# Kernel optimization log

Measured on AMD Instinct MI355X. Metric: run time of the kernel, lower is better.

Reference implementation:

```python
import jax, jax.numpy as jnp
import numpy as np

N, E, D, R, L = 50000, 600000, 64, 65, 2


def setup_inputs() -> dict:
    key = jax.random.key(0)
    ks = jax.random.split(key, 10)
    x = jax.random.normal(ks[0], (N, D), dtype=jnp.float32)
    edge_index = jax.random.randint(ks[1], (2, E), 0, N, dtype=jnp.int64)
    edge_type = jax.random.randint(ks[2], (E,), 0, R, dtype=jnp.int64)
    s = 1.0 / np.sqrt(D)
    W = jax.random.normal(ks[3], (L, R, D, D), dtype=jnp.float32) * s
    root = jax.random.normal(ks[4], (L, D, D), dtype=jnp.float32) * s
    bias = jax.random.normal(ks[5], (L, D), dtype=jnp.float32) * 0.01
    res_W = jax.random.normal(ks[6], (L, D, D), dtype=jnp.float32) * s
    res_b = jax.random.normal(ks[7], (L, D), dtype=jnp.float32) * 0.01
    return {"x": x, "edge_index": edge_index, "edge_type": edge_type,
            "W": W, "root": root, "bias": bias, "res_W": res_W, "res_b": res_b}


def _rgcn_conv(x, src, dst, edge_type, W_r, W_root, b):
    # PyG RGCNConv (num_bases=None, aggr='mean'):
    #   out_i = x_i @ W_root + b + sum_r mean_{j in N_r(i)} (x_j @ W_r)
    # mean is linear, so aggregate raw features per (node, relation) first,
    # then apply the per-relation transform once per node.
    n, d = x.shape
    r = W_r.shape[0]
    seg = dst * r + edge_type                       # [E]
    msg = x[src]                                    # [E, D] gather
    agg = jax.ops.segment_sum(msg, seg, num_segments=n * r).reshape(n, r, d)
    cnt = jax.ops.segment_sum(jnp.ones((msg.shape[0],), x.dtype), seg,
                              num_segments=n * r).reshape(n, r, 1)
    mean = agg / jnp.maximum(cnt, 1.0)              # [N, R, D]
    out = jnp.einsum('nrd,rdk->nk', mean, W_r)
    return out + x @ W_root + b


def reference(x, edge_index, edge_type, W, root, bias, res_W, res_b):
    src, dst = edge_index[0], edge_index[1]
    h = x
    for l in range(W.shape[0]):
        conv = _rgcn_conv(h, src, dst, edge_type, W[l], root[l], bias[l])
        conv = jax.nn.relu(conv)
        # dropout: identity in eval mode
        res = jax.nn.relu(h @ res_W[l] + res_b[l])
        h = conv + res
    return h
```

## Files before the change

kernel.cpp:

```cpp
#include <hip/hip_runtime.h>


constexpr int NN  = 50000;
constexpr int EE  = 600000;
constexpr int DIM = 64;
constexpr int RR  = 65;
constexpr int CHUNK = 256;
constexpr int MAXCHUNKS = EE / CHUNK + RR + 8;
constexpr int SORT_BS = 4096;
constexpr int NSB = (EE + SORT_BS - 1) / SORT_BS;
constexpr int SCAN_BS = 1024;
constexpr int SCAN_NB = (NN + SCAN_BS - 1) / SCAN_BS;
constexpr int XNB = 64;

typedef __attribute__((ext_vector_type(8))) short short8v;
typedef __attribute__((ext_vector_type(4))) float floatx4;

__device__ inline unsigned short f2bf(float f) {
  unsigned int u = __float_as_uint(f);
  return (unsigned short)((u + 0x7fffu + ((u >> 16) & 1u)) >> 16);
}
__device__ inline float bf2f(unsigned short v) {
  return __uint_as_float(((unsigned int)v) << 16);
}


__global__ __launch_bounds__(256) void hist_k(const int* __restrict__ dst,
                                              const int* __restrict__ et,
                                              int* __restrict__ cnt,
                                              int* __restrict__ deg,
                                              int* __restrict__ bhist, int E) {
  __shared__ int lh[RR];
  for (int i = threadIdx.x; i < RR; i += 256) lh[i] = 0;
  __syncthreads();
  const int base = blockIdx.x * SORT_BS;
  for (int i = threadIdx.x; i < SORT_BS; i += 256) {
    const int e = base + i;
    if (e < E) {
      const int d = dst[e], r = et[e];
      atomicAdd(&lh[r], 1);
      atomicAdd(&cnt[d * RR + r], 1);
      atomicAdd(&deg[d], 1);
    }
  }
  __syncthreads();
  for (int i = threadIdx.x; i < RR; i += 256) bhist[blockIdx.x * RR + i] = lh[i];
}


__global__ __launch_bounds__(1024) void scan1_k(const int* __restrict__ deg,
                                                int* __restrict__ bsum) {
  __shared__ int s[SCAN_BS];
  const int idx = blockIdx.x * SCAN_BS + threadIdx.x;
  s[threadIdx.x] = (idx < NN) ? deg[idx] : 0;
  __syncthreads();
  for (int off = SCAN_BS / 2; off > 0; off >>= 1) {
    if (threadIdx.x < off) s[threadIdx.x] += s[threadIdx.x + off];
    __syncthreads();
  }
  if (threadIdx.x == 0) bsum[blockIdx.x] = s[0];
}

__global__ __launch_bounds__(64) void scan2_k(int* __restrict__ bsum) {
  if (threadIdx.x == 0) {
    int run = 0;
    for (int b = 0; b < SCAN_NB; ++b) { const int v = bsum[b]; bsum[b] = run; run += v; }
  }
}

__global__ __launch_bounds__(1024) void scan3_k(const int* __restrict__ deg,
                                                const int* __restrict__ bsum,
                                                int* __restrict__ rowptr,
                                                int* __restrict__ poscur) {
  __shared__ int s[SCAN_BS];
  const int t = threadIdx.x;
  const int idx = blockIdx.x * SCAN_BS + t;
  const int v = (idx < NN) ? deg[idx] : 0;
  s[t] = v;
  __syncthreads();
  for (int off = 1; off < SCAN_BS; off <<= 1) {
    const int u = (t >= off) ? s[t - off] : 0;
    __syncthreads();
    s[t] += u;
    __syncthreads();
  }
  const int excl = bsum[blockIdx.x] + s[t] - v;
  if (idx < NN) { rowptr[idx] = excl; poscur[idx] = excl; }
  if (idx == NN - 1) rowptr[NN] = EE;
}

__global__ __launch_bounds__(128) void scan_type_k(const int* __restrict__ bhist,
                                                   int* __restrict__ boff,
                                                   int4* __restrict__ chunkArr,
                                                   int* __restrict__ nchunks) {
  __shared__ int total[RR], tptr[RR + 1], chbase[RR + 1];
  const int t = threadIdx.x;
  if (t < RR) {
    int s = 0;
    for (int b = 0; b < NSB; ++b) s += bhist[b * RR + t];
    total[t] = s;
  }
  __syncthreads();
  if (t == 0) {
    int run = 0, crun = 0;
    for (int r = 0; r < RR; ++r) {
      tptr[r] = run;   run  += total[r];
      chbase[r] = crun; crun += (total[r] + CHUNK - 1) / CHUNK;
    }
    tptr[RR] = run; chbase[RR] = crun;
    *nchunks = crun;
  }
  __syncthreads();
  if (t < RR) {
    int run = tptr[t];
    for (int b = 0; b < NSB; ++b) { boff[b * RR + t] = run; run += bhist[b * RR + t]; }
    const int nc = (total[t] + CHUNK - 1) / CHUNK;
    for (int i = 0; i < nc; ++i) {
      const int beg = tptr[t] + i * CHUNK;
      chunkArr[chbase[t] + i] = make_int4(beg, min(beg + CHUNK, tptr[t] + total[t]), t, 0);
    }
  }
}

__global__ __launch_bounds__(256) void scatter_k(const int* __restrict__ src,
                                                 const int* __restrict__ dst,
                                                 const int* __restrict__ et,
                                                 const int* __restrict__ cnt,
                                                 const int* __restrict__ boff,
                                                 int* __restrict__ poscur,
                                                 int* __restrict__ osrc,
                                                 int* __restrict__ opos,
                                                 float* __restrict__ oscale, int E) {
  __shared__ int cur[RR];
  for (int i = threadIdx.x; i < RR; i += 256) cur[i] = boff[blockIdx.x * RR + i];
  __syncthreads();
  const int base = blockIdx.x * SORT_BS;
  for (int i = threadIdx.x; i < SORT_BS; i += 256) {
    const int e = base + i;
    if (e < E) {
      const int s = src[e], d = dst[e], r = et[e];
      const int q = atomicAdd(&cur[r], 1);
      const int p = atomicAdd(&poscur[d], 1);
      osrc[q] = s;
      opos[q] = p;
      oscale[q] = 1.0f / (float)cnt[d * RR + r];
    }
  }
}


__global__ __launch_bounds__(256) void cvtw_k(const float* __restrict__ W,
                                              unsigned short* __restrict__ WT) {
  const int tid = blockIdx.x * 256 + threadIdx.x;
  const int total4 = 2 * RR * DIM * DIM / 4;
  if (tid >= total4) return;
  const int base = tid * 4;
  const int mat = base >> 12;
  const int rem = base & 4095;
  const int k = rem >> 6, c0 = rem & 63;
  const float4 v = *reinterpret_cast<const float4*>(W + base);
  unsigned short* o = WT + (size_t)mat * 4096;
  o[(c0 + 0) * 64 + k] = f2bf(v.x);
  o[(c0 + 1) * 64 + k] = f2bf(v.y);
  o[(c0 + 2) * 64 + k] = f2bf(v.z);
  o[(c0 + 3) * 64 + k] = f2bf(v.w);
}

__global__ __launch_bounds__(256) void cvth_k(const float* __restrict__ h,
                                              unsigned short* __restrict__ hbf) {
  const int tid = blockIdx.x * 256 + threadIdx.x;
  if (tid * 8 >= NN * DIM) return;
  const float4 v0 = reinterpret_cast<const float4*>(h)[tid * 2];
  const float4 v1 = reinterpret_cast<const float4*>(h)[tid * 2 + 1];
  ushort4 a, b;
  a.x = f2bf(v0.x); a.y = f2bf(v0.y); a.z = f2bf(v0.z); a.w = f2bf(v0.w);
  b.x = f2bf(v1.x); b.y = f2bf(v1.y); b.z = f2bf(v1.z); b.w = f2bf(v1.w);
  reinterpret_cast<ushort4*>(hbf)[tid * 2] = a;
  reinterpret_cast<ushort4*>(hbf)[tid * 2 + 1] = b;
}


__global__ __launch_bounds__(256) void msgm_k(const unsigned short* __restrict__ hbf,
                                              const int* __restrict__ osrc,
                                              const int* __restrict__ opos,
                                              const float* __restrict__ oscale,
                                              const unsigned short* __restrict__ WT,
                                              const int4* __restrict__ chunkArr,
                                              const int* __restrict__ nchunks,
                                              unsigned short* __restrict__ m) {
  const int ci = blockIdx.x;
  if (ci >= *nchunks) return;
  const int4 c = chunkArr[ci];
  const int beg = c.x, end = c.y, rel = c.z;

  __shared__ unsigned short Wl[DIM][72];
  {
    const float4* s4 = reinterpret_cast<const float4*>(WT + (size_t)rel * 4096);
#pragma unroll
    for (int it = 0; it < 2; ++it) {
      const int seg = threadIdx.x + it * 256;
      const int row = seg >> 3, s8 = seg & 7;
      *reinterpret_cast<float4*>(&Wl[row][s8 * 8]) = s4[seg];
    }
  }
  __syncthreads();

  const int w  = threadIdx.x >> 6;
  const int l  = threadIdx.x & 63;
  const int lr = l & 15, lq = l >> 4;

  const int ebase = beg + w * 64;
  if (ebase >= end) return;

  short8v a[4][2];
#pragma unroll
  for (int ct = 0; ct < 4; ++ct)
#pragma unroll
    for (int kk = 0; kk < 2; ++kk)
      a[ct][kk] = *reinterpret_cast<const short8v*>(&Wl[ct * 16 + lr][kk * 32 + lq * 8]);

  short8v b[4][2];
  int eidx[4];
#pragma unroll
  for (int et = 0; et < 4; ++et) {
    eidx[et] = ebase + et * 16 + lr;
    const int e = min(eidx[et], end - 1);
    const int s = osrc[e];
    const unsigned short* hp = hbf + (size_t)s * DIM;
    b[et][0] = *reinterpret_cast<const short8v*>(hp + lq * 8);
    b[et][1] = *reinterpret_cast<const short8v*>(hp + 32 + lq * 8);
  }

  floatx4 acc[4][4];
#pragma unroll
  for (int ct = 0; ct < 4; ++ct)
#pragma unroll
    for (int et = 0; et < 4; ++et)
      acc[ct][et] = (floatx4){0.f, 0.f, 0.f, 0.f};

#pragma unroll
  for (int kk = 0; kk < 2; ++kk)
#pragma unroll
    for (int ct = 0; ct < 4; ++ct)
#pragma unroll
      for (int et = 0; et < 4; ++et)
        acc[ct][et] = __builtin_amdgcn_mfma_f32_16x16x32_bf16(a[ct][kk], b[et][kk],
                                                              acc[ct][et], 0, 0, 0);

#pragma unroll
  for (int et = 0; et < 4; ++et) {
    const int e = eidx[et];
    if (e < end) {
      const float sc = oscale[e];
      unsigned short* op = m + (size_t)opos[e] * DIM;
#pragma unroll
      for (int ct = 0; ct < 4; ++ct) {
        ushort4 o;
        o.x = f2bf(acc[ct][et][0] * sc);
        o.y = f2bf(acc[ct][et][1] * sc);
        o.z = f2bf(acc[ct][et][2] * sc);
        o.w = f2bf(acc[ct][et][3] * sc);
        *reinterpret_cast<ushort4*>(op + ct * 16 + lq * 4) = o;
      }
    }
  }
}

__global__ __launch_bounds__(256) void msg_k(const float* __restrict__ h,
                                             const int* __restrict__ osrc,
                                             const int* __restrict__ opos,
                                             const float* __restrict__ oscale,
                                             const float* __restrict__ W,
                                             const int4* __restrict__ chunkArr,
                                             const int* __restrict__ nchunks,
                                             unsigned short* __restrict__ m) {
  const int ci = blockIdx.x;
  if (ci >= *nchunks) return;
  const int4 c = chunkArr[ci];
  const int beg = c.x, end = c.y, rel = c.z;

  __shared__ float Wlds[DIM * DIM];
  const float* Wg = W + (size_t)rel * (DIM * DIM);
#pragma unroll
  for (int i = 0; i < 4; ++i)
    *reinterpret_cast<float4*>(&Wlds[i * 1024 + threadIdx.x * 4]) =
        *reinterpret_cast<const float4*>(Wg + i * 1024 + threadIdx.x * 4);
  __syncthreads();

  const int g = threadIdx.x >> 4, li = threadIdx.x & 15;
  __shared__ float xs[16][4][68];

  for (int b = 0; b < 4; ++b) {
    const int e0 = beg + g * 16 + b * 4;
    const int nvalid = min(4, end - e0);
    if (nvalid <= 0) continue;

#pragma unroll
    for (int r = 0; r < 4; ++r) {
      const int e = e0 + ((r < nvalid) ? r : (nvalid - 1));
      const int s = osrc[e];
      *reinterpret_cast<float4*>(&xs[g][r][li * 4]) =
          *reinterpret_cast<const float4*>(h + (size_t)s * DIM + li * 4);
    }

    float acc[4][4];
#pragma unroll
    for (int r = 0; r < 4; ++r) { acc[r][0] = 0.f; acc[r][1] = 0.f; acc[r][2] = 0.f; acc[r][3] = 0.f; }

#pragma unroll 8
    for (int k = 0; k < DIM; ++k) {
      const float4 w = *reinterpret_cast<const float4*>(&Wlds[k * DIM + li * 4]);
#pragma unroll
      for (int r = 0; r < 4; ++r) {
        const float xv = xs[g][r][k];
        acc[r][0] += xv * w.x; acc[r][1] += xv * w.y;
        acc[r][2] += xv * w.z; acc[r][3] += xv * w.w;
      }
    }

    for (int r = 0; r < nvalid; ++r) {
      const int e = e0 + r;
      const float sc = oscale[e];
      ushort4 o;
      o.x = f2bf(acc[r][0] * sc); o.y = f2bf(acc[r][1] * sc);
      o.z = f2bf(acc[r][2] * sc); o.w = f2bf(acc[r][3] * sc);
      *reinterpret_cast<ushort4*>(m + (size_t)opos[e] * DIM + li * 4) = o;
    }
  }
}

__global__ __launch_bounds__(256) void xform_k(const float* __restrict__ h,
                                               const float* __restrict__ root,
                                               const float* __restrict__ bias,
                                               const float* __restrict__ rw,
                                               const float* __restrict__ rb,
                                               float* __restrict__ rt,
                                               float* __restrict__ rs, int N) {
  __shared__ float Wl0[DIM * DIM];
  __shared__ float Wl1[DIM * DIM];
  __shared__ float xs[XNB][68];
#pragma unroll
  for (int i = 0; i < 4; ++i) {
    reinterpret_cast<float4*>(Wl0)[threadIdx.x + i * 256] =
        reinterpret_cast<const float4*>(root)[threadIdx.x + i * 256];
    reinterpret_cast<float4*>(Wl1)[threadIdx.x + i * 256] =
        reinterpret_cast<const float4*>(rw)[threadIdx.x + i * 256];
  }

  const int g = threadIdx.x >> 4, li = threadIdx.x & 15;
  const int base = blockIdx.x * XNB;
#pragma unroll
  for (int r = 0; r < 4; ++r) {
    const int n = base + g * 4 + r;
    float4 v = make_float4(0.f, 0.f, 0.f, 0.f);
    if (n < N) v = *reinterpret_cast<const float4*>(h + (size_t)n * DIM + li * 4);
    *reinterpret_cast<float4*>(&xs[g * 4 + r][li * 4]) = v;
  }
  __syncthreads();

  float aR[4][4], aS[4][4];
#pragma unroll
  for (int r = 0; r < 4; ++r)
#pragma unroll
    for (int q = 0; q < 4; ++q) { aR[r][q] = 0.f; aS[r][q] = 0.f; }

#pragma unroll 4
  for (int k = 0; k < DIM; ++k) {
    const float4 wr = *reinterpret_cast<const float4*>(&Wl0[k * DIM + li * 4]);
    const float4 wv = *reinterpret_cast<const float4*>(&Wl1[k * DIM + li * 4]);
#pragma unroll
    for (int r = 0; r < 4; ++r) {
      const float xv = xs[g * 4 + r][k];
      aR[r][0] += xv * wr.x; aR[r][1] += xv * wr.y; aR[r][2] += xv * wr.z; aR[r][3] += xv * wr.w;
      aS[r][0] += xv * wv.x; aS[r][1] += xv * wv.y; aS[r][2] += xv * wv.z; aS[r][3] += xv * wv.w;
    }
  }

  const float4 bv = reinterpret_cast<const float4*>(bias)[li];
  const float4 cv = reinterpret_cast<const float4*>(rb)[li];
#pragma unroll
  for (int r = 0; r < 4; ++r) {
    const int n = base + g * 4 + r;
    if (n < N) {
      *reinterpret_cast<float4*>(rt + (size_t)n * DIM + li * 4) =
          make_float4(aR[r][0] + bv.x, aR[r][1] + bv.y, aR[r][2] + bv.z, aR[r][3] + bv.w);
      *reinterpret_cast<float4*>(rs + (size_t)n * DIM + li * 4) =
          make_float4(fmaxf(aS[r][0] + cv.x, 0.f), fmaxf(aS[r][1] + cv.y, 0.f),
                      fmaxf(aS[r][2] + cv.z, 0.f), fmaxf(aS[r][3] + cv.w, 0.f));
    }
  }
}

__global__ __launch_bounds__(256) void gather2_k(const unsigned short* __restrict__ m,
                                                 const int* __restrict__ rowptr,
                                                 const float* __restrict__ rt,
                                                 const float* __restrict__ rs,
                                                 float* __restrict__ hout, int N) {
  const int g = threadIdx.x >> 4, li = threadIdx.x & 15;
  const int n = blockIdx.x * 16 + g;
  if (n >= N) return;

  float a0 = 0.f, a1 = 0.f, a2 = 0.f, a3 = 0.f;
  const int jb = rowptr[n], je = rowptr[n + 1];
  int j = jb;
  for (; j + 4 <= je; j += 4) {
    const ushort4 v0 = *reinterpret_cast<const ushort4*>(m + (size_t)(j + 0) * DIM + li * 4);
    const ushort4 v1 = *reinterpret_cast<const ushort4*>(m + (size_t)(j + 1) * DIM + li * 4);
    const ushort4 v2 = *reinterpret_cast<const ushort4*>(m + (size_t)(j + 2) * DIM + li * 4);
    const ushort4 v3 = *reinterpret_cast<const ushort4*>(m + (size_t)(j + 3) * DIM + li * 4);
    a0 += bf2f(v0.x) + bf2f(v1.x) + bf2f(v2.x) + bf2f(v3.x);
    a1 += bf2f(v0.y) + bf2f(v1.y) + bf2f(v2.y) + bf2f(v3.y);
    a2 += bf2f(v0.z) + bf2f(v1.z) + bf2f(v2.z) + bf2f(v3.z);
    a3 += bf2f(v0.w) + bf2f(v1.w) + bf2f(v2.w) + bf2f(v3.w);
  }
  for (; j < je; ++j) {
    const ushort4 v = *reinterpret_cast<const ushort4*>(m + (size_t)j * DIM + li * 4);
    a0 += bf2f(v.x); a1 += bf2f(v.y); a2 += bf2f(v.z); a3 += bf2f(v.w);
  }

  const float4 t = *reinterpret_cast<const float4*>(rt + (size_t)n * DIM + li * 4);
  const float4 s = *reinterpret_cast<const float4*>(rs + (size_t)n * DIM + li * 4);
  *reinterpret_cast<float4*>(hout + (size_t)n * DIM + li * 4) =
      make_float4(fmaxf(a0 + t.x, 0.f) + s.x, fmaxf(a1 + t.y, 0.f) + s.y,
                  fmaxf(a2 + t.z, 0.f) + s.z, fmaxf(a3 + t.w, 0.f) + s.w);
}

__global__ __launch_bounds__(256) void gather_k(const float* __restrict__ hin,
                                                const unsigned short* __restrict__ m,
                                                const int* __restrict__ rowptr,
                                                const float* __restrict__ root,
                                                const float* __restrict__ bias,
                                                const float* __restrict__ rw,
                                                const float* __restrict__ rb,
                                                float* __restrict__ hout, int N) {
  __shared__ float xs[16][68];
  const int g = threadIdx.x >> 4, li = threadIdx.x & 15;
  const int n = blockIdx.x * 16 + g;
  if (n >= N) return;

  *reinterpret_cast<float4*>(&xs[g][li * 4]) =
      *reinterpret_cast<const float4*>(hin + (size_t)n * DIM + li * 4);

  float a0 = 0.f, a1 = 0.f, a2 = 0.f, a3 = 0.f;
  const int jb = rowptr[n], je = rowptr[n + 1];
  for (int j = jb; j < je; ++j) {
    const ushort4 mv = *reinterpret_cast<const ushort4*>(m + (size_t)j * DIM + li * 4);
    a0 += bf2f(mv.x); a1 += bf2f(mv.y); a2 += bf2f(mv.z); a3 += bf2f(mv.w);
  }

  float r0 = 0.f, r1 = 0.f, r2 = 0.f, r3 = 0.f;
  float s0 = 0.f, s1 = 0.f, s2 = 0.f, s3 = 0.f;
#pragma unroll 8
  for (int k = 0; k < DIM; ++k) {
    const float hd = xs[g][k];
    const float4 w = *reinterpret_cast<const float4*>(root + k * DIM + li * 4);
    const float4 v = *reinterpret_cast<const float4*>(rw + k * DIM + li * 4);
    r0 += hd * w.x; r1 += hd * w.y; r2 += hd * w.z; r3 += hd * w.w;
    s0 += hd * v.x; s1 += hd * v.y; s2 += hd * v.z; s3 += hd * v.w;
  }
  const float4 b = *reinterpret_cast<const float4*>(bias + li * 4);
  const float4 cc = *reinterpret_cast<const float4*>(rb + li * 4);
  float o0 = fmaxf(a0 + r0 + b.x, 0.f) + fmaxf(s0 + cc.x, 0.f);
  float o1 = fmaxf(a1 + r1 + b.y, 0.f) + fmaxf(s1 + cc.y, 0.f);
  float o2 = fmaxf(a2 + r2 + b.z, 0.f) + fmaxf(s2 + cc.z, 0.f);
  float o3 = fmaxf(a3 + r3 + b.w, 0.f) + fmaxf(s3 + cc.w, 0.f);
  *reinterpret_cast<float4*>(hout + (size_t)n * DIM + li * 4) = make_float4(o0, o1, o2, o3);
}


__global__ __launch_bounds__(256) void count_k(const int* __restrict__ dst,
                                               const int* __restrict__ et,
                                               int* __restrict__ cnt, int E) {
  int e = blockIdx.x * 256 + threadIdx.x;
  if (e < E) atomicAdd(&cnt[dst[e] * RR + et[e]], 1);
}

__global__ __launch_bounds__(256) void edge_k(const float* __restrict__ h,
                                              const int* __restrict__ src,
                                              const int* __restrict__ dst,
                                              const int* __restrict__ et,
                                              const float* __restrict__ W,
                                              const int* __restrict__ cnt,
                                              float* __restrict__ accum, int E) {
  __shared__ float xs[16][68];
  const int g = threadIdx.x >> 4, li = threadIdx.x & 15;
  const int e = blockIdx.x * 16 + g;
  if (e >= E) return;
  const int s = src[e], d = dst[e], t = et[e];
  *reinterpret_cast<float4*>(&xs[g][li * 4]) =
      *reinterpret_cast<const float4*>(h + (size_t)s * DIM + li * 4);
  const float* Wt = W + (size_t)t * (DIM * DIM) + li * 4;
  float a0 = 0.f, a1 = 0.f, a2 = 0.f, a3 = 0.f;
#pragma unroll 8
  for (int k = 0; k < DIM; ++k) {
    const float xd = xs[g][k];
    const float4 w = *reinterpret_cast<const float4*>(Wt + k * DIM);
    a0 += xd * w.x; a1 += xd * w.y; a2 += xd * w.z; a3 += xd * w.w;
  }
  const float sc = 1.0f / (float)cnt[d * RR + t];
  float* o = accum + (size_t)d * DIM + li * 4;
  unsafeAtomicAdd(o + 0, a0 * sc);
  unsafeAtomicAdd(o + 1, a1 * sc);
  unsafeAtomicAdd(o + 2, a2 * sc);
  unsafeAtomicAdd(o + 3, a3 * sc);
}

__global__ __launch_bounds__(256) void node_k(const float* __restrict__ h,
                                              const float* __restrict__ root,
                                              const float* __restrict__ bias,
                                              const float* __restrict__ rw,
                                              const float* __restrict__ rb,
                                              float* __restrict__ io, int N) {
  __shared__ float xs[16][68];
  const int g = threadIdx.x >> 4, li = threadIdx.x & 15;
  const int n = blockIdx.x * 16 + g;
  if (n >= N) return;
  *reinterpret_cast<float4*>(&xs[g][li * 4]) =
      *reinterpret_cast<const float4*>(h + (size_t)n * DIM + li * 4);
  float r0 = 0.f, r1 = 0.f, r2 = 0.f, r3 = 0.f;
  float s0 = 0.f, s1 = 0.f, s2 = 0.f, s3 = 0.f;
#pragma unroll 8
  for (int k = 0; k < DIM; ++k) {
    const float hd = xs[g][k];
    const float4 w = *reinterpret_cast<const float4*>(root + k * DIM + li * 4);
    const float4 v = *reinterpret_cast<const float4*>(rw + k * DIM + li * 4);
    r0 += hd * w.x; r1 += hd * w.y; r2 += hd * w.z; r3 += hd * w.w;
    s0 += hd * v.x; s1 += hd * v.y; s2 += hd * v.z; s3 += hd * v.w;
  }
  float* o = io + (size_t)n * DIM + li * 4;
  const float4 acc = *reinterpret_cast<const float4*>(o);
  const float4 b = *reinterpret_cast<const float4*>(bias + li * 4);
  const float4 c = *reinterpret_cast<const float4*>(rb + li * 4);
  float o0 = fmaxf(acc.x + r0 + b.x, 0.f) + fmaxf(s0 + c.x, 0.f);
  float o1 = fmaxf(acc.y + r1 + b.y, 0.f) + fmaxf(s1 + c.y, 0.f);
  float o2 = fmaxf(acc.z + r2 + b.z, 0.f) + fmaxf(s2 + c.z, 0.f);
  float o3 = fmaxf(acc.w + r3 + b.w, 0.f) + fmaxf(s3 + c.w, 0.f);
  *reinterpret_cast<float4*>(o) = make_float4(o0, o1, o2, o3);
}


extern "C" void kernel_launch(void* const* d_in, const int* in_sizes, int n_in,
                              void* d_out, int out_size, void* d_ws, size_t ws_size,
                              hipStream_t stream) {
  const float* x    = (const float*)d_in[0];
  const int*   ei   = (const int*)d_in[1];
  const int*   et   = (const int*)d_in[2];
  const float* W    = (const float*)d_in[3];
  const float* root = (const float*)d_in[4];
  const float* bias = (const float*)d_in[5];
  const float* resW = (const float*)d_in[6];
  const float* resb = (const float*)d_in[7];
  float* out = (float*)d_out;

  const int* src = ei;
  const int* dstp = ei + EE;

  char* ws = (char*)d_ws;
  size_t off = 0;
  auto take = [&](size_t bytes) -> void* {
    void* p = ws + off;
    off = (off + bytes + 255) & ~(size_t)255;
    return p;
  };
  unsigned short* m = (unsigned short*)take((size_t)EE * DIM * sizeof(unsigned short));
  float* h1      = (float*)take((size_t)NN * DIM * sizeof(float));
  int* deg       = (int*)take((size_t)NN * sizeof(int));
  int* rowptr    = (int*)take((size_t)(NN + 1) * sizeof(int));
  int* poscur    = (int*)take((size_t)NN * sizeof(int));
  int* bhist     = (int*)take((size_t)NSB * RR * sizeof(int));
  int* boff      = (int*)take((size_t)NSB * RR * sizeof(int));
  int* bsum      = (int*)take((size_t)SCAN_NB * sizeof(int));
  int* osrc      = (int*)take((size_t)EE * sizeof(int));
  int* opos      = (int*)take((size_t)EE * sizeof(int));
  float* oscale  = (float*)take((size_t)EE * sizeof(float));
  int4* chunkArr = (int4*)take((size_t)MAXCHUNKS * sizeof(int4));
  int* nchunks   = (int*)take(256);
  const size_t base_off = off;
  float* rt      = (float*)take((size_t)NN * DIM * sizeof(float));
  float* rs      = (float*)take((size_t)NN * DIM * sizeof(float));
  const size_t t1_off = off;
  unsigned short* hbf = (unsigned short*)take((size_t)NN * DIM * sizeof(unsigned short));
  unsigned short* wbt = (unsigned short*)take((size_t)2 * RR * DIM * DIM * sizeof(unsigned short));
  const size_t mfma_off = off;
  int* cnt       = (int*)m;

  if (base_off <= ws_size) {
    hipMemsetAsync(cnt, 0, (size_t)NN * RR * sizeof(int), stream);
    hipMemsetAsync(deg, 0, (size_t)NN * sizeof(int), stream);

    hist_k<<<NSB, 256, 0, stream>>>(dstp, et, cnt, deg, bhist, EE);
    scan1_k<<<SCAN_NB, 1024, 0, stream>>>(deg, bsum);
    scan2_k<<<1, 64, 0, stream>>>(bsum);
    scan3_k<<<SCAN_NB, 1024, 0, stream>>>(deg, bsum, rowptr, poscur);
    scan_type_k<<<1, 128, 0, stream>>>(bhist, boff, chunkArr, nchunks);
    scatter_k<<<NSB, 256, 0, stream>>>(src, dstp, et, cnt, boff, poscur,
                                       osrc, opos, oscale, EE);

    const int XG = (NN + XNB - 1) / XNB;
    const int HG = (NN * DIM / 8 + 255) / 256;
    if (mfma_off <= ws_size) {
      cvtw_k<<<(2 * RR * DIM * DIM / 4 + 255) / 256, 256, 0, stream>>>(W, wbt);
      cvth_k<<<HG, 256, 0, stream>>>(x, hbf);
      msgm_k<<<MAXCHUNKS, 256, 0, stream>>>(hbf, osrc, opos, oscale, wbt, chunkArr, nchunks, m);
      xform_k<<<XG, 256, 0, stream>>>(x, root, bias, resW, resb, rt, rs, NN);
      gather2_k<<<(NN + 15) / 16, 256, 0, stream>>>(m, rowptr, rt, rs, h1, NN);
      cvth_k<<<HG, 256, 0, stream>>>(h1, hbf);
      msgm_k<<<MAXCHUNKS, 256, 0, stream>>>(hbf, osrc, opos, oscale,
                                            wbt + (size_t)RR * DIM * DIM, chunkArr, nchunks, m);
      xform_k<<<XG, 256, 0, stream>>>(h1, root + DIM * DIM, bias + DIM,
                                      resW + DIM * DIM, resb + DIM, rt, rs, NN);
      gather2_k<<<(NN + 15) / 16, 256, 0, stream>>>(m, rowptr, rt, rs, out, NN);
    } else if (t1_off <= ws_size) {
      msg_k<<<MAXCHUNKS, 256, 0, stream>>>(x, osrc, opos, oscale, W, chunkArr, nchunks, m);
      xform_k<<<XG, 256, 0, stream>>>(x, root, bias, resW, resb, rt, rs, NN);
      gather2_k<<<(NN + 15) / 16, 256, 0, stream>>>(m, rowptr, rt, rs, h1, NN);
      msg_k<<<MAXCHUNKS, 256, 0, stream>>>(h1, osrc, opos, oscale,
                                           W + (size_t)RR * DIM * DIM, chunkArr, nchunks, m);
      xform_k<<<XG, 256, 0, stream>>>(h1, root + DIM * DIM, bias + DIM,
                                      resW + DIM * DIM, resb + DIM, rt, rs, NN);
      gather2_k<<<(NN + 15) / 16, 256, 0, stream>>>(m, rowptr, rt, rs, out, NN);
    } else {
      msg_k<<<MAXCHUNKS, 256, 0, stream>>>(x, osrc, opos, oscale, W, chunkArr, nchunks, m);
      gather_k<<<(NN + 15) / 16, 256, 0, stream>>>(x, m, rowptr, root, bias, resW, resb, h1, NN);
      msg_k<<<MAXCHUNKS, 256, 0, stream>>>(h1, osrc, opos, oscale,
                                           W + (size_t)RR * DIM * DIM, chunkArr, nchunks, m);
      gather_k<<<(NN + 15) / 16, 256, 0, stream>>>(h1, m, rowptr, root + DIM * DIM, bias + DIM,
                                                   resW + DIM * DIM, resb + DIM, out, NN);
    }
  } else {
    int* fcnt = (int*)ws;
    float* fh1 = (float*)(ws + (size_t)NN * RR * sizeof(int));
    hipMemsetAsync(fcnt, 0, (size_t)NN * RR * sizeof(int), stream);
    hipMemsetAsync(fh1, 0, (size_t)NN * DIM * sizeof(float), stream);
    hipMemsetAsync(out, 0, (size_t)NN * DIM * sizeof(float), stream);
    count_k<<<(EE + 255) / 256, 256, 0, stream>>>(dstp, et, fcnt, EE);
    edge_k<<<(EE + 15) / 16, 256, 0, stream>>>(x, src, dstp, et, W, fcnt, fh1, EE);
    node_k<<<(NN + 15) / 16, 256, 0, stream>>>(x, root, bias, resW, resb, fh1, NN);
    edge_k<<<(EE + 15) / 16, 256, 0, stream>>>(fh1, src, dstp, et,
                                               W + (size_t)RR * DIM * DIM, fcnt, out, EE);
    node_k<<<(NN + 15) / 16, 256, 0, stream>>>(fh1, root + DIM * DIM, bias + DIM,
                                               resW + DIM * DIM, resb + DIM, out, NN);
  }
}
```

Measured before the change: 273.0 us.

## Fuse bf16 cast into xform, split histogram, and transpose count layout

Removes the separate cvth_k conversion kernels by having xform_k write the bf16 copy of h from its shared-memory tile, and reorders launches so xform runs before msgm. The combined histogram kernel is split into a flat per-edge count kernel and a per-block relation histogram. The per-(node,relation) count array becomes relation-major, and node degree is derived in scan1_k by summing 65 counts instead of a separate atomic. Sort block size is halved and block width raised to 512. The aim is fewer launches and fewer global atomics, at the cost of 65 strided reads per node in scan1 and an extra pass over edge types.

```diff
diff --git a/kernel.cpp b/kernel.cpp
--- a/kernel.cpp
+++ b/kernel.cpp
@@ -7,7 +7,7 @@
 constexpr int RR  = 65;
 constexpr int CHUNK = 256;
 constexpr int MAXCHUNKS = EE / CHUNK + RR + 8;
-constexpr int SORT_BS = 4096;
+constexpr int SORT_BS = 2048;
 constexpr int NSB = (EE + SORT_BS - 1) / SORT_BS;
 constexpr int SCAN_BS = 1024;
 constexpr int SCAN_NB = (NN + SCAN_BS - 1) / SCAN_BS;
@@ -25,34 +25,40 @@
 }
 
 
-__global__ __launch_bounds__(256) void hist_k(const int* __restrict__ dst,
-                                              const int* __restrict__ et,
-                                              int* __restrict__ cnt,
-                                              int* __restrict__ deg,
-                                              int* __restrict__ bhist, int E) {
+__global__ __launch_bounds__(512) void cnt_k(const int* __restrict__ dst,
+                                             const int* __restrict__ et,
+                                             int* __restrict__ cnt, int E) {
+  const int e = blockIdx.x * 512 + threadIdx.x;
+  if (e < E) atomicAdd(&cnt[et[e] * NN + dst[e]], 1);
+}
+
+__global__ __launch_bounds__(512) void bhist_k(const int* __restrict__ et,
+                                               int* __restrict__ bhist, int E) {
   __shared__ int lh[RR];
-  for (int i = threadIdx.x; i < RR; i += 256) lh[i] = 0;
+  for (int i = threadIdx.x; i < RR; i += 512) lh[i] = 0;
   __syncthreads();
   const int base = blockIdx.x * SORT_BS;
-  for (int i = threadIdx.x; i < SORT_BS; i += 256) {
+  for (int i = threadIdx.x; i < SORT_BS; i += 512) {
     const int e = base + i;
-    if (e < E) {
-      const int d = dst[e], r = et[e];
-      atomicAdd(&lh[r], 1);
-      atomicAdd(&cnt[d * RR + r], 1);
-      atomicAdd(&deg[d], 1);
-    }
-  }
-  __syncthreads();
-  for (int i = threadIdx.x; i < RR; i += 256) bhist[blockIdx.x * RR + i] = lh[i];
-}
-
-
-__global__ __launch_bounds__(1024) void scan1_k(const int* __restrict__ deg,
+    if (e < E) atomicAdd(&lh[et[e]], 1);
+  }
+  __syncthreads();
+  for (int i = threadIdx.x; i < RR; i += 512) bhist[blockIdx.x * RR + i] = lh[i];
+}
+
+
+__global__ __launch_bounds__(1024) void scan1_k(const int* __restrict__ cnt,
+                                                int* __restrict__ deg,
                                                 int* __restrict__ bsum) {
   __shared__ int s[SCAN_BS];
   const int idx = blockIdx.x * SCAN_BS + threadIdx.x;
-  s[threadIdx.x] = (idx < NN) ? deg[idx] : 0;
+  int d = 0;
+  if (idx < NN) {
+#pragma unroll 13
+    for (int r = 0; r < RR; ++r) d += cnt[r * NN + idx];
+    deg[idx] = d;
+  }
+  s[threadIdx.x] = d;
   __syncthreads();
   for (int off = SCAN_BS / 2; off > 0; off >>= 1) {
     if (threadIdx.x < off) s[threadIdx.x] += s[threadIdx.x + off];
@@ -122,7 +128,7 @@
   }
 }
 
-__global__ __launch_bounds__(256) void scatter_k(const int* __restrict__ src,
+__global__ __launch_bounds__(512) void scatter_k(const int* __restrict__ src,
                                                  const int* __restrict__ dst,
                                                  const int* __restrict__ et,
                                                  const int* __restrict__ cnt,
@@ -132,10 +138,10 @@
                                                  int* __restrict__ opos,
                                                  float* __restrict__ oscale, int E) {
   __shared__ int cur[RR];
-  for (int i = threadIdx.x; i < RR; i += 256) cur[i] = boff[blockIdx.x * RR + i];
+  for (int i = threadIdx.x; i < RR; i += 512) cur[i] = boff[blockIdx.x * RR + i];
   __syncthreads();
   const int base = blockIdx.x * SORT_BS;
-  for (int i = threadIdx.x; i < SORT_BS; i += 256) {
+  for (int i = threadIdx.x; i < SORT_BS; i += 512) {
     const int e = base + i;
     if (e < E) {
       const int s = src[e], d = dst[e], r = et[e];
@@ -143,7 +149,7 @@
       const int p = atomicAdd(&poscur[d], 1);
       osrc[q] = s;
       opos[q] = p;
-      oscale[q] = 1.0f / (float)cnt[d * RR + r];
+      oscale[q] = 1.0f / (float)cnt[r * NN + d];
     }
   }
 }
@@ -166,19 +172,6 @@
   o[(c0 + 3) * 64 + k] = f2bf(v.w);
 }
 
-__global__ __launch_bounds__(256) void cvth_k(const float* __restrict__ h,
-                                              unsigned short* __restrict__ hbf) {
-  const int tid = blockIdx.x * 256 + threadIdx.x;
-  if (tid * 8 >= NN * DIM) return;
-  const float4 v0 = reinterpret_cast<const float4*>(h)[tid * 2];
-  const float4 v1 = reinterpret_cast<const float4*>(h)[tid * 2 + 1];
-  ushort4 a, b;
-  a.x = f2bf(v0.x); a.y = f2bf(v0.y); a.z = f2bf(v0.z); a.w = f2bf(v0.w);
-  b.x = f2bf(v1.x); b.y = f2bf(v1.y); b.z = f2bf(v1.z); b.w = f2bf(v1.w);
-  reinterpret_cast<ushort4*>(hbf)[tid * 2] = a;
-  reinterpret_cast<ushort4*>(hbf)[tid * 2 + 1] = b;
-}
-
 
 __global__ __launch_bounds__(256) void msgm_k(const unsigned short* __restrict__ hbf,
                                               const int* __restrict__ osrc,
@@ -335,7 +328,8 @@
                                                const float* __restrict__ rw,
                                                const float* __restrict__ rb,
                                                float* __restrict__ rt,
-                                               float* __restrict__ rs, int N) {
+                                               float* __restrict__ rs,
+                                               unsigned short* __restrict__ hbf, int N) {
   __shared__ float Wl0[DIM * DIM];
   __shared__ float Wl1[DIM * DIM];
   __shared__ float xs[XNB][68];
@@ -357,6 +351,19 @@
     *reinterpret_cast<float4*>(&xs[g * 4 + r][li * 4]) = v;
   }
   __syncthreads();
+
+  if (hbf != nullptr) {
+#pragma unroll
+    for (int r = 0; r < 4; ++r) {
+      const int n = base + g * 4 + r;
+      if (n < N) {
+        const float4 v = *reinterpret_cast<const float4*>(&xs[g * 4 + r][li * 4]);
+        ushort4 o;
+        o.x = f2bf(v.x); o.y = f2bf(v.y); o.z = f2bf(v.z); o.w = f2bf(v.w);
+        *reinterpret_cast<ushort4*>(hbf + (size_t)n * DIM + li * 4) = o;
+      }
+    }
+  }
 
   float aR[4][4], aS[4][4];
 #pragma unroll
@@ -586,38 +593,35 @@
 
   if (base_off <= ws_size) {
     hipMemsetAsync(cnt, 0, (size_t)NN * RR * sizeof(int), stream);
-    hipMemsetAsync(deg, 0, (size_t)NN * sizeof(int), stream);
-
-    hist_k<<<NSB, 256, 0, stream>>>(dstp, et, cnt, deg, bhist, EE);
-    scan1_k<<<SCAN_NB, 1024, 0, stream>>>(deg, bsum);
+
+    cnt_k<<<(EE + 511) / 512, 512, 0, stream>>>(dstp, et, cnt, EE);
+    bhist_k<<<NSB, 512, 0, stream>>>(et, bhist, EE);
+    scan1_k<<<SCAN_NB, 1024, 0, stream>>>(cnt, deg, bsum);
     scan2_k<<<1, 64, 0, stream>>>(bsum);
     scan3_k<<<SCAN_NB, 1024, 0, stream>>>(deg, bsum, rowptr, poscur);
     scan_type_k<<<1, 128, 0, stream>>>(bhist, boff, chunkArr, nchunks);
-    scatter_k<<<NSB, 256, 0, stream>>>(src, dstp, et, cnt, boff, poscur,
+    scatter_k<<<NSB, 512, 0, stream>>>(src, dstp, et, cnt, boff, poscur,
                                        osrc, opos, oscale, EE);
 
     const int XG = (NN + XNB - 1) / XNB;
-    const int HG = (NN * DIM / 8 + 255) / 256;
     if (mfma_off <= ws_size) {
       cvtw_k<<<(2 * RR * DIM * DIM / 4 + 255) / 256, 256, 0, stream>>>(W, wbt);
-      cvth_k<<<HG, 256, 0, stream>>>(x, hbf);
+      xform_k<<<XG, 256, 0, stream>>>(x, root, bias, resW, resb, rt, rs, hbf, NN);
       msgm_k<<<MAXCHUNKS, 256, 0, stream>>>(hbf, osrc, opos, oscale, wbt, chunkArr, nchunks, m);
-      xform_k<<<XG, 256, 0, stream>>>(x, root, bias, resW, resb, rt, rs, NN);
       gather2_k<<<(NN + 15) / 16, 256, 0, stream>>>(m, rowptr, rt, rs, h1, NN);
-      cvth_k<<<HG, 256, 0, stream>>>(h1, hbf);
+      xform_k<<<XG, 256, 0, stream>>>(h1, root + DIM * DIM, bias + DIM,
+                                      resW + DIM * DIM, resb + DIM, rt, rs, hbf, NN);
       msgm_k<<<MAXCHUNKS, 256, 0, stream>>>(hbf, osrc, opos, oscale,
                                             wbt + (size_t)RR * DIM * DIM, chunkArr, nchunks, m);
-      xform_k<<<XG, 256, 0, stream>>>(h1, root + DIM * DIM, bias + DIM,
-                                      resW + DIM * DIM, resb + DIM, rt, rs, NN);
       gather2_k<<<(NN + 15) / 16, 256, 0, stream>>>(m, rowptr, rt, rs, out, NN);
     } else if (t1_off <= ws_size) {
       msg_k<<<MAXCHUNKS, 256, 0, stream>>>(x, osrc, opos, oscale, W, chunkArr, nchunks, m);
-      xform_k<<<XG, 256, 0, stream>>>(x, root, bias, resW, resb, rt, rs, NN);
+      xform_k<<<XG, 256, 0, stream>>>(x, root, bias, resW, resb, rt, rs, nullptr, NN);
       gather2_k<<<(NN + 15) / 16, 256, 0, stream>>>(m, rowptr, rt, rs, h1, NN);
       msg_k<<<MAXCHUNKS, 256, 0, stream>>>(h1, osrc, opos, oscale,
                                            W + (size_t)RR * DIM * DIM, chunkArr, nchunks, m);
       xform_k<<<XG, 256, 0, stream>>>(h1, root + DIM * DIM, bias + DIM,
-                                      resW + DIM * DIM, resb + DIM, rt, rs, NN);
+                                      resW + DIM * DIM, resb + DIM, rt, rs, nullptr, NN);
       gather2_k<<<(NN + 15) / 16, 256, 0, stream>>>(m, rowptr, rt, rs, out, NN);
     } else {
       msg_k<<<MAXCHUNKS, 256, 0, stream>>>(x, osrc, opos, oscale, W, chunkArr, nchunks, m);
```

Result: no change. 273.0 us (+0.0%).
